# Kernel tuning notes

Measured on AMD Instinct MI355X. Metric: run time of the kernel, lower is better.

Reference implementation:

```python
import jax, jax.numpy as jnp
import numpy as np

N = 50000      # nodes
E = 1600000    # edges (avg degree 32)
F = 64         # input node features
H = 128        # GAT hidden dim (heads=1)
A = 16         # action dim
ED = 2         # edge feature dim


def setup_inputs() -> dict:
    key = jax.random.key(0)
    ks = jax.random.split(key, 20)
    def w(k, shape, fan_in):
        return jax.random.normal(k, shape, jnp.float32) * (1.0 / np.sqrt(fan_in))
    return {
        "x": jax.random.normal(ks[0], (N, F), jnp.float32),
        "edge_index": jax.random.randint(ks[1], (2, E), 0, N, dtype=jnp.int32),
        "edge_attr": jax.random.normal(ks[2], (E, ED), jnp.float32),
        # GATConv layer 1 (F -> H)
        "W1": w(ks[3], (F, H), F),
        "We1": w(ks[4], (ED, H), ED),
        "asrc1": w(ks[5], (H,), H),
        "adst1": w(ks[6], (H,), H),
        "aedge1": w(ks[7], (H,), H),
        "b1": jnp.zeros((H,), jnp.float32),
        # GATConv layer 2 (H -> H)
        "W2": w(ks[8], (H, H), H),
        "We2": w(ks[9], (ED, H), ED),
        "asrc2": w(ks[10], (H,), H),
        "adst2": w(ks[11], (H,), H),
        "aedge2": w(ks[12], (H,), H),
        "b2": jnp.zeros((H,), jnp.float32),
        # final head
        "Wfc": w(ks[13], (H, A), H),
        "bfc": jnp.zeros((A,), jnp.float32),
    }


def _gat_layer(x, src, dst, ea, W, We, a_s, a_d, a_e, b, n):
    """PyG GATConv, heads=1: gather -> attn logits -> segment softmax -> scatter-add."""
    h = x @ W                      # [n, H]
    he = ea @ We                   # [E', H]
    logits = jax.nn.leaky_relu(
        (h * a_s).sum(-1)[src] + (h * a_d).sum(-1)[dst] + (he * a_e).sum(-1),
        negative_slope=0.2,
    )                              # [E']
    m = jax.ops.segment_max(logits, dst, num_segments=n)
    p = jnp.exp(logits - m[dst])
    denom = jax.ops.segment_sum(p, dst, num_segments=n)
    alpha = p / (denom[dst] + 1e-16)
    out = jax.ops.segment_sum(h[src] * alpha[:, None], dst, num_segments=n)
    return out + b


def reference(x, edge_index, edge_attr, W1, We1, asrc1, adst1, aedge1, b1,
              W2, We2, asrc2, adst2, aedge2, b2, Wfc, bfc):
    n = x.shape[0]
    src0, dst0 = edge_index[0], edge_index[1]
    # add_self_loops=True with fill_value='mean': self-loop edge_attr is the
    # mean of incoming edge_attr per destination node (0 if no incoming edges)
    cnt = jax.ops.segment_sum(jnp.ones_like(dst0, dtype=edge_attr.dtype), dst0, num_segments=n)
    ea_mean = jax.ops.segment_sum(edge_attr, dst0, num_segments=n) / jnp.maximum(cnt, 1.0)[:, None]
    loops = jnp.arange(n, dtype=src0.dtype)
    src = jnp.concatenate([src0, loops])
    dst = jnp.concatenate([dst0, loops])
    ea = jnp.concatenate([edge_attr, ea_mean], axis=0)

    h = jax.nn.relu(_gat_layer(x, src, dst, ea, W1, We1, asrc1, adst1, aedge1, b1, n))
    h = jax.nn.relu(_gat_layer(h, src, dst, ea, W2, We2, asrc2, adst2, aedge2, b2, n))
    pooled = h.mean(axis=0)        # [H]
    return jnp.tanh(pooled @ Wfc + bfc)
```

## Files before the change

kernel.cpp:

```cpp
#include <hip/hip_runtime.h>
#include <math.h>

#define H_DIM 128
#define BWID 128
#define BMAX 512
#define CHUNK 4096

typedef int v4i __attribute__((ext_vector_type(4)));

__global__ void prep_kernel(const float* __restrict__ We1, const float* __restrict__ ae1,
                            const float* __restrict__ We2, const float* __restrict__ ae2,
                            const float* __restrict__ W1, const float* __restrict__ as1,
                            const float* __restrict__ ad1,
                            const float* __restrict__ W2, const float* __restrict__ as2,
                            const float* __restrict__ ad2,
                            float* __restrict__ c, float* __restrict__ vs1,
                            float* __restrict__ vd1, float* __restrict__ vs2,
                            float* __restrict__ vd2) {
    int t = threadIdx.x;
    if (t < 64) {
        float s = 0.f, d = 0.f;
        for (int h = 0; h < 128; ++h) {
            float w = W1[t * 128 + h];
            s += w * as1[h];
            d += w * ad1[h];
        }
        vs1[t] = s; vd1[t] = d;
    } else if (t < 192) {
        int k = t - 64;
        float s = 0.f, d = 0.f;
        for (int h = 0; h < 128; ++h) {
            float w = W2[k * 128 + h];
            s += w * as2[h];
            d += w * ad2[h];
        }
        vs2[k] = s; vd2[k] = d;
    } else {
        int l = t - 192;
        float a1x = ae1[l], a1y = ae1[l + 64];
        float a2x = ae2[l], a2y = ae2[l + 64];
        float v0 = We1[l] * a1x + We1[l + 64] * a1y;
        float v1 = We1[128 + l] * a1x + We1[192 + l] * a1y;
        float v2 = We2[l] * a2x + We2[l + 64] * a2y;
        float v3 = We2[128 + l] * a2x + We2[192 + l] * a2y;
        for (int off = 32; off; off >>= 1) {
            v0 += __shfl_xor(v0, off);
            v1 += __shfl_xor(v1, off);
            v2 += __shfl_xor(v2, off);
            v3 += __shfl_xor(v3, off);
        }
        if (l == 0) { c[0] = v0; c[1] = v1; c[2] = v2; c[3] = v3; }
    }
}

__global__ __launch_bounds__(256) void count_kernel(const int* __restrict__ ei,
                                                    int* __restrict__ gcnt, int E, int B) {
    __shared__ int hist[BMAX];
    int tid = threadIdx.x;
    for (int i = tid; i < B; i += 256) hist[i] = 0;
    __syncthreads();
    int lo = blockIdx.x * CHUNK, hi = min(lo + CHUNK, E);
    for (int e = lo + tid; e < hi; e += 256)
        atomicAdd(&hist[ei[E + e] >> 7], 1);
    __syncthreads();
    for (int i = tid; i < B; i += 256)
        if (hist[i]) atomicAdd(&gcnt[i], hist[i]);
}

__global__ void bscan_kernel(const int* __restrict__ gcnt, int* __restrict__ bstart,
                             int* __restrict__ gcur, int* __restrict__ rowptr,
                             int B, int n, int E) {
    __shared__ int s[BMAX];
    int t = threadIdx.x;
    int v0 = (t < B) ? gcnt[t] : 0;
    s[t] = v0;
    __syncthreads();
    for (int off = 1; off < BMAX; off <<= 1) {
        int v = (t >= off) ? s[t - off] : 0;
        __syncthreads();
        s[t] += v;
        __syncthreads();
    }
    if (t < B) {
        int excl = s[t] - v0;
        bstart[t] = excl;
        gcur[t] = excl;
    }
    if (t == 0) { bstart[B] = E; rowptr[n] = E; }
}

__global__ __launch_bounds__(256) void bin_kernel(const int* __restrict__ ei,
                                                  const float* __restrict__ ea,
                                                  const float* __restrict__ cvec,
                                                  int* __restrict__ gcur,
                                                  int4* __restrict__ binned, int E, int B) {
    __shared__ int cnt[BMAX];
    __shared__ int base[BMAX];
    int tid = threadIdx.x;
    for (int i = tid; i < B; i += 256) cnt[i] = 0;
    __syncthreads();
    int lo = blockIdx.x * CHUNK, hi = min(lo + CHUNK, E);
    for (int e = lo + tid; e < hi; e += 256)
        atomicAdd(&cnt[ei[E + e] >> 7], 1);
    __syncthreads();
    for (int i = tid; i < B; i += 256) {
        int c = cnt[i];
        base[i] = c ? atomicAdd(&gcur[i], c) : 0;
        cnt[i] = 0;
    }
    __syncthreads();
    float c0 = cvec[0], c1 = cvec[1], c2 = cvec[2], c3 = cvec[3];
    for (int e = lo + tid; e < hi; e += 256) {
        int s = ei[e], d = ei[E + e];
        float2 v = ((const float2*)ea)[e];
        float d1 = c0 * v.x + c1 * v.y;
        float d2 = c2 * v.x + c3 * v.y;
        int b = d >> 7;
        int loc = atomicAdd(&cnt[b], 1);
        binned[(size_t)(base[b] + loc)] = make_int4(s, d, __float_as_int(d1), __float_as_int(d2));
    }
}

__global__ __launch_bounds__(256) void build_kernel(const int* __restrict__ bstart,
                                                    const int4* __restrict__ binned,
                                                    int* __restrict__ rowptr,
                                                    int4* __restrict__ csr, int n) {
    __shared__ int cnt[BWID];
    __shared__ int sc[BWID];
    __shared__ int cur[BWID];
    int b = blockIdx.x, tid = threadIdx.x;
    int d0 = b << 7;
    int lo = bstart[b], hi = bstart[b + 1];
    if (tid < BWID) cnt[tid] = 0;
    __syncthreads();
    for (int k = lo + tid; k < hi; k += 256)
        atomicAdd(&cnt[binned[k].y & (BWID - 1)], 1);
    __syncthreads();
    if (tid < BWID) sc[tid] = cnt[tid];
    __syncthreads();
    for (int off = 1; off < BWID; off <<= 1) {
        int v = (tid < BWID && tid >= off) ? sc[tid - off] : 0;
        __syncthreads();
        if (tid < BWID) sc[tid] += v;
        __syncthreads();
    }
    if (tid < BWID) {
        int excl = sc[tid] - cnt[tid];
        cur[tid] = lo + excl;
        int d = d0 + tid;
        if (d < n) rowptr[d] = lo + excl;
    }
    __syncthreads();
    for (int k = lo + tid; k < hi; k += 256) {
        int4 e = binned[k];
        int slot = atomicAdd(&cur[e.y & (BWID - 1)], 1);
        csr[slot] = make_int4(e.x, e.z, e.w, 0);
    }
}

__global__ void hshd64_kernel(const float* __restrict__ x, const float* __restrict__ vs,
                              const float* __restrict__ vd, float* __restrict__ hs,
                              float* __restrict__ hd, int n) {
    int w = (blockIdx.x * blockDim.x + threadIdx.x) >> 6;
    int lane = threadIdx.x & 63;
    if (w >= n) return;
    float xv = x[(size_t)w * 64 + lane];
    float ss = xv * vs[lane];
    float sd = xv * vd[lane];
    for (int off = 32; off; off >>= 1) {
        ss += __shfl_xor(ss, off);
        sd += __shfl_xor(sd, off);
    }
    if (lane == 0) { hs[w] = ss; hd[w] = sd; }
}

__global__ __launch_bounds__(256) void agg64_kernel(
        const int* __restrict__ rowptr, const int4* __restrict__ csr,
        const float* __restrict__ hs, const float* __restrict__ hd,
        const float* __restrict__ feat, float* __restrict__ t_out, int n) {
    int w = (blockIdx.x * blockDim.x + threadIdx.x) >> 6;
    int lane = threadIdx.x & 63;
    if (w >= n) return;
    int beg = rowptr[w], end = rowptr[w + 1];
    int len = end - beg;
    float hdv = hd[w], hsw = hs[w];
    int g = lane >> 4;
    int c16 = lane & 15;
    float4 acc = make_float4(0.f, 0.f, 0.f, 0.f);
    float m, scale, lself;

    if (len <= 64) {
        bool valid = lane < len;
        int4 c4 = valid ? csr[beg + lane] : make_int4(0, 0, 0, 0);
        float ed = valid ? __int_as_float(c4.y) : 0.f;
        float l = hs[c4.x] + hdv + ed;
        l = (l >= 0.f) ? l : 0.2f * l;
        float mymax = valid ? l : -1e30f;
        float edsum = ed;
        for (int off = 32; off; off >>= 1) {
            mymax = fmaxf(mymax, __shfl_xor(mymax, off));
            edsum += __shfl_xor(edsum, off);
        }
        lself = hsw + hdv + edsum / fmaxf((float)len, 1.0f);
        lself = (lself >= 0.f) ? lself : 0.2f * lself;
        m = fmaxf(mymax, lself);
        float p = valid ? __expf(l - m) : 0.f;
        float psum = p;
        for (int off = 32; off; off >>= 1) psum += __shfl_xor(psum, off);
        psum += __expf(lself - m);
        scale = 1.f / (psum + 1e-16f);
        float pn = p * scale;
        int src = c4.x;
        for (int j = g; j < len; j += 4) {
            float a = __shfl(pn, j);
            int sj = __shfl(src, j);
            const float4 hv = *(const float4*)&feat[(size_t)sj * 64 + c16 * 4];
            acc.x += a * hv.x; acc.y += a * hv.y; acc.z += a * hv.z; acc.w += a * hv.w;
        }
    } else {
        float mymax = -1e30f, edsum = 0.f;
        for (int base = beg; base < end; base += 64) {
            int k = base + lane;
            if (k < end) {
                int4 c4 = csr[k];
                float ed = __int_as_float(c4.y);
                edsum += ed;
                float l = hs[c4.x] + hdv + ed;
                l = (l >= 0.f) ? l : 0.2f * l;
                mymax = fmaxf(mymax, l);
            }
        }
        for (int off = 32; off; off >>= 1) {
            mymax = fmaxf(mymax, __shfl_xor(mymax, off));
            edsum += __shfl_xor(edsum, off);
        }
        lself = hsw + hdv + edsum / fmaxf((float)len, 1.0f);
        lself = (lself >= 0.f) ? lself : 0.2f * lself;
        m = fmaxf(mymax, lself);
        float psum = 0.f;
        for (int base = beg; base < end; base += 64) {
            int k = base + lane;
            if (k < end) {
                int4 c4 = csr[k];
                float l = hs[c4.x] + hdv + __int_as_float(c4.y);
                l = (l >= 0.f) ? l : 0.2f * l;
                psum += __expf(l - m);
            }
        }
        for (int off = 32; off; off >>= 1) psum += __shfl_xor(psum, off);
        psum += __expf(lself - m);
        scale = 1.f / (psum + 1e-16f);
        for (int base = beg; base < end; base += 64) {
            int k = base + lane;
            float pn = 0.f; int src = 0;
            if (k < end) {
                int4 c4 = csr[k];
                float l = hs[c4.x] + hdv + __int_as_float(c4.y);
                l = (l >= 0.f) ? l : 0.2f * l;
                pn = __expf(l - m) * scale;
                src = c4.x;
            }
            int cl = min(end - base, 64);
            for (int j = g; j < cl; j += 4) {
                float a = __shfl(pn, j);
                int sj = __shfl(src, j);
                const float4 hv = *(const float4*)&feat[(size_t)sj * 64 + c16 * 4];
                acc.x += a * hv.x; acc.y += a * hv.y; acc.z += a * hv.z; acc.w += a * hv.w;
            }
        }
    }
    if (g == 0) {
        float a = __expf(lself - m) * scale;
        const float4 hv = *(const float4*)&feat[(size_t)w * 64 + c16 * 4];
        acc.x += a * hv.x; acc.y += a * hv.y; acc.z += a * hv.z; acc.w += a * hv.w;
    }
    float4 p1, p2, p3;
    p1.x = __shfl(acc.x, c16 + 16); p1.y = __shfl(acc.y, c16 + 16);
    p1.z = __shfl(acc.z, c16 + 16); p1.w = __shfl(acc.w, c16 + 16);
    p2.x = __shfl(acc.x, c16 + 32); p2.y = __shfl(acc.y, c16 + 32);
    p2.z = __shfl(acc.z, c16 + 32); p2.w = __shfl(acc.w, c16 + 32);
    p3.x = __shfl(acc.x, c16 + 48); p3.y = __shfl(acc.y, c16 + 48);
    p3.z = __shfl(acc.z, c16 + 48); p3.w = __shfl(acc.w, c16 + 48);
    if (lane < 16) {
        float4 o;
        o.x = acc.x + p1.x + p2.x + p3.x;
        o.y = acc.y + p1.y + p2.y + p3.y;
        o.z = acc.z + p1.z + p2.z + p3.z;
        o.w = acc.w + p1.w + p2.w + p3.w;
        *(float4*)&t_out[(size_t)w * 64 + c16 * 4] = o;
    }
}

__global__ __launch_bounds__(256) void agg128_kernel(
        const int* __restrict__ rowptr, const int4* __restrict__ csr,
        const float* __restrict__ hs, const float* __restrict__ hd,
        const float* __restrict__ feat, float* __restrict__ t_out, int n) {
    int w = (blockIdx.x * blockDim.x + threadIdx.x) >> 6;
    int lane = threadIdx.x & 63;
    if (w >= n) return;
    int beg = rowptr[w], end = rowptr[w + 1];
    int len = end - beg;
    float hdv = hd[w], hsw = hs[w];
    int half = lane >> 5;
    int col = lane & 31;
    float4 acc = make_float4(0.f, 0.f, 0.f, 0.f);
    float m, scale, lself;

    if (len <= 64) {
        bool valid = lane < len;
        int4 c4 = valid ? csr[beg + lane] : make_int4(0, 0, 0, 0);
        float ed = valid ? __int_as_float(c4.z) : 0.f;
        float l = hs[c4.x] + hdv + ed;
        l = (l >= 0.f) ? l : 0.2f * l;
        float mymax = valid ? l : -1e30f;
        float edsum = ed;
        for (int off = 32; off; off >>= 1) {
            mymax = fmaxf(mymax, __shfl_xor(mymax, off));
            edsum += __shfl_xor(edsum, off);
        }
        lself = hsw + hdv + edsum / fmaxf((float)len, 1.0f);
        lself = (lself >= 0.f) ? lself : 0.2f * lself;
        m = fmaxf(mymax, lself);
        float p = valid ? __expf(l - m) : 0.f;
        float psum = p;
        for (int off = 32; off; off >>= 1) psum += __shfl_xor(psum, off);
        psum += __expf(lself - m);
        scale = 1.f / (psum + 1e-16f);
        float pn = p * scale;
        int src = c4.x;
        for (int j = half; j < len; j += 2) {
            float a = __shfl(pn, j);
            int sj = __shfl(src, j);
            const float4 hv = *(const float4*)&feat[(size_t)sj * H_DIM + col * 4];
            acc.x += a * hv.x; acc.y += a * hv.y; acc.z += a * hv.z; acc.w += a * hv.w;
        }
    } else {
        float mymax = -1e30f, edsum = 0.f;
        for (int base = beg; base < end; base += 64) {
            int k = base + lane;
            if (k < end) {
                int4 c4 = csr[k];
                float ed = __int_as_float(c4.z);
                edsum += ed;
                float l = hs[c4.x] + hdv + ed;
                l = (l >= 0.f) ? l : 0.2f * l;
                mymax = fmaxf(mymax, l);
            }
        }
        for (int off = 32; off; off >>= 1) {
            mymax = fmaxf(mymax, __shfl_xor(mymax, off));
            edsum += __shfl_xor(edsum, off);
        }
        lself = hsw + hdv + edsum / fmaxf((float)len, 1.0f);
        lself = (lself >= 0.f) ? lself : 0.2f * lself;
        m = fmaxf(mymax, lself);
        float psum = 0.f;
        for (int base = beg; base < end; base += 64) {
            int k = base + lane;
            if (k < end) {
                int4 c4 = csr[k];
                float l = hs[c4.x] + hdv + __int_as_float(c4.z);
                l = (l >= 0.f) ? l : 0.2f * l;
                psum += __expf(l - m);
            }
        }
        for (int off = 32; off; off >>= 1) psum += __shfl_xor(psum, off);
        psum += __expf(lself - m);
        scale = 1.f / (psum + 1e-16f);
        for (int base = beg; base < end; base += 64) {
            int k = base + lane;
            float pn = 0.f; int src = 0;
            if (k < end) {
                int4 c4 = csr[k];
                float l = hs[c4.x] + hdv + __int_as_float(c4.z);
                l = (l >= 0.f) ? l : 0.2f * l;
                pn = __expf(l - m) * scale;
                src = c4.x;
            }
            int cl = min(end - base, 64);
            for (int j = half; j < cl; j += 2) {
                float a = __shfl(pn, j);
                int sj = __shfl(src, j);
                const float4 hv = *(const float4*)&feat[(size_t)sj * H_DIM + col * 4];
                acc.x += a * hv.x; acc.y += a * hv.y; acc.z += a * hv.z; acc.w += a * hv.w;
            }
        }
    }
    if (half == 0) {
        float a = __expf(lself - m) * scale;
        const float4 hv = *(const float4*)&feat[(size_t)w * H_DIM + col * 4];
        acc.x += a * hv.x; acc.y += a * hv.y; acc.z += a * hv.z; acc.w += a * hv.w;
    }
    float4 oth;
    oth.x = __shfl(acc.x, col + 32);
    oth.y = __shfl(acc.y, col + 32);
    oth.z = __shfl(acc.z, col + 32);
    oth.w = __shfl(acc.w, col + 32);
    if (half == 0) {
        float4 o;
        o.x = acc.x + oth.x; o.y = acc.y + oth.y;
        o.z = acc.z + oth.z; o.w = acc.w + oth.w;
        *(float4*)&t_out[(size_t)w * H_DIM + col * 4] = o;
    }
}

template <int FIN, bool DO_HSHD>
__global__ __launch_bounds__(256) void gemm_kernel(const float* __restrict__ X,
                                                   const float* __restrict__ W,
                                                   const float* __restrict__ bias,
                                                   const float* __restrict__ vs,
                                                   const float* __restrict__ vd,
                                                   float* __restrict__ Hout,
                                                   float* __restrict__ hs,
                                                   float* __restrict__ hd, int n) {
    __shared__ float xs[32 * FIN];
    int tid = threadIdx.x;
    int r0 = blockIdx.x * 32;
    for (int idx = tid; idx < 32 * FIN; idx += 256) {
        int r = idx / FIN, k = idx - r * FIN;
        int row = r0 + r;
        xs[idx] = (row < n) ? X[(size_t)row * FIN + k] : 0.0f;
    }
    __syncthreads();
    int tcol = tid & 31;
    int trow = tid >> 5;
    float acc[4][4] = {{0.f}};
    const float* wp = W + tcol * 4;
    const float* x0p = &xs[(trow * 4 + 0) * FIN];
    const float* x1p = &xs[(trow * 4 + 1) * FIN];
    const float* x2p = &xs[(trow * 4 + 2) * FIN];
    const float* x3p = &xs[(trow * 4 + 3) * FIN];
#pragma unroll 8
    for (int k = 0; k < FIN; ++k) {
        float4 w4 = *(const float4*)(wp + k * H_DIM);
        float x0 = x0p[k], x1 = x1p[k], x2 = x2p[k], x3 = x3p[k];
        acc[0][0] += x0 * w4.x; acc[0][1] += x0 * w4.y; acc[0][2] += x0 * w4.z; acc[0][3] += x0 * w4.w;
        acc[1][0] += x1 * w4.x; acc[1][1] += x1 * w4.y; acc[1][2] += x1 * w4.z; acc[1][3] += x1 * w4.w;
        acc[2][0] += x2 * w4.x; acc[2][1] += x2 * w4.y; acc[2][2] += x2 * w4.z; acc[2][3] += x2 * w4.w;
        acc[3][0] += x3 * w4.x; acc[3][1] += x3 * w4.y; acc[3][2] += x3 * w4.z; acc[3][3] += x3 * w4.w;
    }
    float4 b4 = *(const float4*)&bias[tcol * 4];
    float4 vs4, vd4;
    if (DO_HSHD) {
        vs4 = *(const float4*)&vs[tcol * 4];
        vd4 = *(const float4*)&vd[tcol * 4];
    }
#pragma unroll
    for (int r = 0; r < 4; ++r) {
        int row = r0 + trow * 4 + r;
        float4 o;
        o.x = fmaxf(acc[r][0] + b4.x, 0.f);
        o.y = fmaxf(acc[r][1] + b4.y, 0.f);
        o.z = fmaxf(acc[r][2] + b4.z, 0.f);
        o.w = fmaxf(acc[r][3] + b4.w, 0.f);
        if (row < n) *(float4*)&Hout[(size_t)row * H_DIM + tcol * 4] = o;
        if (DO_HSHD) {
            float ss = o.x * vs4.x + o.y * vs4.y + o.z * vs4.z + o.w * vs4.w;
            float sd = o.x * vd4.x + o.y * vd4.y + o.z * vd4.z + o.w * vd4.w;
            for (int off = 16; off; off >>= 1) {
                ss += __shfl_xor(ss, off);
                sd += __shfl_xor(sd, off);
            }
            if (tcol == 0 && row < n) { hs[row] = ss; hd[row] = sd; }
        }
    }
}

__global__ void pool_kernel(const float* __restrict__ hmat, float* __restrict__ pooled,
                            int n) {
    __shared__ float red[256];
    int col = threadIdx.x & 127;
    int half = threadIdx.x >> 7;
    int rows_per_block = (n + gridDim.x - 1) / gridDim.x;
    int r0 = blockIdx.x * rows_per_block;
    int r1 = min(r0 + rows_per_block, n);
    float s = 0.f;
    for (int r = r0 + half; r < r1; r += 2) s += hmat[(size_t)r * H_DIM + col];
    red[threadIdx.x] = s;
    __syncthreads();
    if (half == 0) atomicAdd(&pooled[col], red[threadIdx.x] + red[threadIdx.x + 128]);
}

__global__ void final_kernel(const float* __restrict__ pooled, const float* __restrict__ Wfc,
                             const float* __restrict__ bfc, float* __restrict__ out, int n) {
    int t = threadIdx.x;
    if (t >= 16) return;
    float inv_n = 1.0f / (float)n;
    float s = 0.f;
    for (int j = 0; j < 128; ++j) s += pooled[j] * inv_n * Wfc[j * 16 + t];
    out[t] = tanhf(s + bfc[t]);
}

extern "C" void kernel_launch(void* const* d_in, const int* in_sizes, int n_in,
                              void* d_out, int out_size, void* d_ws, size_t ws_size,
                              hipStream_t stream) {
    const float* x   = (const float*)d_in[0];
    const int*   ei  = (const int*)d_in[1];
    const float* ea  = (const float*)d_in[2];
    const float* W1  = (const float*)d_in[3];
    const float* We1 = (const float*)d_in[4];
    const float* as1 = (const float*)d_in[5];
    const float* ad1 = (const float*)d_in[6];
    const float* ae1 = (const float*)d_in[7];
    const float* b1  = (const float*)d_in[8];
    const float* W2  = (const float*)d_in[9];
    const float* We2 = (const float*)d_in[10];
    const float* as2 = (const float*)d_in[11];
    const float* ad2 = (const float*)d_in[12];
    const float* ae2 = (const float*)d_in[13];
    const float* b2  = (const float*)d_in[14];
    const float* Wfc = (const float*)d_in[15];
    const float* bfc = (const float*)d_in[16];
    float* out = (float*)d_out;

    const int n = in_sizes[0] / 64;
    const int E = in_sizes[1] / 2;
    const int B = (n + BWID - 1) / BWID;

    size_t o = 0;
    auto alloc = [&](size_t count) { size_t r = o; o += (count + 63) & ~(size_t)63; return r; };
    size_t o_gcnt   = alloc(BMAX);
    size_t o_bstart = alloc(BMAX + 1);
    size_t o_gcur   = alloc(BMAX);
    size_t o_rowptr = alloc(n + 1);
    size_t o_csr    = alloc(4 * (size_t)E);
    size_t o_hs     = alloc(n);
    size_t o_hd     = alloc(n);
    size_t o_bufA   = alloc((size_t)n * H_DIM);
    size_t o_bufB   = alloc((size_t)n * H_DIM);
    size_t o_c      = alloc(4);
    size_t o_vs1    = alloc(64);
    size_t o_vd1    = alloc(64);
    size_t o_vs2    = alloc(128);
    size_t o_vd2    = alloc(128);
    size_t o_pool   = alloc(128);
    (void)ws_size;
    int4* binned = (int4*)((float*)d_ws + o_bufA);

    float* wsf = (float*)d_ws;
    hipMemsetAsync(wsf + o_gcnt, 0, BMAX * sizeof(int), stream);
    hipMemsetAsync(wsf + o_pool, 0, 128 * sizeof(float), stream);

    prep_kernel<<<1, 256, 0, stream>>>(We1, ae1, We2, ae2, W1, as1, ad1, W2, as2, ad2,
        wsf + o_c, wsf + o_vs1, wsf + o_vd1, wsf + o_vs2, wsf + o_vd2);

    int ebg = (E + CHUNK - 1) / CHUNK;
    count_kernel<<<ebg, 256, 0, stream>>>(ei, (int*)(wsf + o_gcnt), E, B);
    bscan_kernel<<<1, BMAX, 0, stream>>>((int*)(wsf + o_gcnt), (int*)(wsf + o_bstart),
        (int*)(wsf + o_gcur), (int*)(wsf + o_rowptr), B, n, E);
    bin_kernel<<<ebg, 256, 0, stream>>>(ei, ea, wsf + o_c, (int*)(wsf + o_gcur),
        binned, E, B);
    build_kernel<<<B, 256, 0, stream>>>((int*)(wsf + o_bstart), binned,
        (int*)(wsf + o_rowptr), (int4*)(wsf + o_csr), n);

    int wgrid = (n + 3) / 4;

    hshd64_kernel<<<wgrid, 256, 0, stream>>>(x, wsf + o_vs1, wsf + o_vd1,
        wsf + o_hs, wsf + o_hd, n);
    agg64_kernel<<<wgrid, 256, 0, stream>>>((int*)(wsf + o_rowptr), (const int4*)(wsf + o_csr),
        wsf + o_hs, wsf + o_hd, x, wsf + o_bufB, n);
    gemm_kernel<64, true><<<(n + 31) / 32, 256, 0, stream>>>(wsf + o_bufB, W1, b1,
        wsf + o_vs2, wsf + o_vd2, wsf + o_bufA, wsf + o_hs, wsf + o_hd, n);

    agg128_kernel<<<wgrid, 256, 0, stream>>>((int*)(wsf + o_rowptr), (const int4*)(wsf + o_csr),
        wsf + o_hs, wsf + o_hd, wsf + o_bufA, wsf + o_bufB, n);
    gemm_kernel<128, false><<<(n + 31) / 32, 256, 0, stream>>>(wsf + o_bufB, W2, b2,
        nullptr, nullptr, wsf + o_bufA, nullptr, nullptr, n);

    pool_kernel<<<256, 256, 0, stream>>>(wsf + o_bufA, wsf + o_pool, n);
    final_kernel<<<1, 64, 0, stream>>>(wsf + o_pool, Wfc, bfc, out, n);
}
```

Before: 445.9 us.

## Split layer-2 aggregation into column passes with precomputed attention weights

```diff
diff --git a/kernel.cpp b/kernel.cpp
--- a/kernel.cpp
+++ b/kernel.cpp
@@ -402,6 +402,159 @@
         o.z = acc.z + oth.z; o.w = acc.w + oth.w;
         *(float4*)&t_out[(size_t)w * H_DIM + col * 4] = o;
     }
+}
+
+__global__ __launch_bounds__(256) void agg128a_kernel(
+        const int* __restrict__ rowptr, const int4* __restrict__ csr,
+        const float* __restrict__ hs, const float* __restrict__ hd,
+        const float* __restrict__ feat, float* __restrict__ t_out,
+        uint2* __restrict__ apack, float* __restrict__ aself, int n) {
+    int w = (blockIdx.x * blockDim.x + threadIdx.x) >> 6;
+    int lane = threadIdx.x & 63;
+    if (w >= n) return;
+    int beg = rowptr[w], end = rowptr[w + 1];
+    int len = end - beg;
+    float hdv = hd[w], hsw = hs[w];
+    int half = lane >> 5;
+    int c32 = lane & 31;
+    float acc = 0.f;
+    float m, scale, lself;
+
+    if (len <= 64) {
+        bool valid = lane < len;
+        int4 c4 = valid ? csr[beg + lane] : make_int4(0, 0, 0, 0);
+        float ed = valid ? __int_as_float(c4.z) : 0.f;
+        float l = hs[c4.x] + hdv + ed;
+        l = (l >= 0.f) ? l : 0.2f * l;
+        float mymax = valid ? l : -1e30f;
+        float edsum = ed;
+        for (int off = 32; off; off >>= 1) {
+            mymax = fmaxf(mymax, __shfl_xor(mymax, off));
+            edsum += __shfl_xor(edsum, off);
+        }
+        lself = hsw + hdv + edsum / fmaxf((float)len, 1.0f);
+        lself = (lself >= 0.f) ? lself : 0.2f * lself;
+        m = fmaxf(mymax, lself);
+        float p = valid ? __expf(l - m) : 0.f;
+        float psum = p;
+        for (int off = 32; off; off >>= 1) psum += __shfl_xor(psum, off);
+        psum += __expf(lself - m);
+        scale = 1.f / (psum + 1e-16f);
+        float pn = p * scale;
+        int src = c4.x;
+        if (valid) apack[beg + lane] = make_uint2((unsigned)src, (unsigned)__float_as_int(pn));
+        for (int j = half; j < len; j += 2) {
+            float a = __shfl(pn, j);
+            int sj = __shfl(src, j);
+            acc += a * feat[(size_t)sj * H_DIM + c32];
+        }
+    } else {
+        float mymax = -1e30f, edsum = 0.f;
+        for (int base = beg; base < end; base += 64) {
+            int k = base + lane;
+            if (k < end) {
+                int4 c4 = csr[k];
+                float ed = __int_as_float(c4.z);
+                edsum += ed;
+                float l = hs[c4.x] + hdv + ed;
+                l = (l >= 0.f) ? l : 0.2f * l;
+                mymax = fmaxf(mymax, l);
+            }
+        }
+        for (int off = 32; off; off >>= 1) {
+            mymax = fmaxf(mymax, __shfl_xor(mymax, off));
+            edsum += __shfl_xor(edsum, off);
+        }
+        lself = hsw + hdv + edsum / fmaxf((float)len, 1.0f);
+        lself = (lself >= 0.f) ? lself : 0.2f * lself;
+        m = fmaxf(mymax, lself);
+        float psum = 0.f;
+        for (int base = beg; base < end; base += 64) {
+            int k = base + lane;
+            if (k < end) {
+                int4 c4 = csr[k];
+                float l = hs[c4.x] + hdv + __int_as_float(c4.z);
+                l = (l >= 0.f) ? l : 0.2f * l;
+                psum += __expf(l - m);
+            }
+        }
+        for (int off = 32; off; off >>= 1) psum += __shfl_xor(psum, off);
+        psum += __expf(lself - m);
+        scale = 1.f / (psum + 1e-16f);
+        for (int base = beg; base < end; base += 64) {
+            int k = base + lane;
+            float pn = 0.f; int src = 0;
+            if (k < end) {
+                int4 c4 = csr[k];
+                float l = hs[c4.x] + hdv + __int_as_float(c4.z);
+                l = (l >= 0.f) ? l : 0.2f * l;
+                pn = __expf(l - m) * scale;
+                src = c4.x;
+                apack[k] = make_uint2((unsigned)src, (unsigned)__float_as_int(pn));
+            }
+            int cl = min(end - base, 64);
+            for (int j = half; j < cl; j += 2) {
+                float a = __shfl(pn, j);
+                int sj = __shfl(src, j);
+                acc += a * feat[(size_t)sj * H_DIM + c32];
+            }
+        }
+    }
+    float aslf = __expf(lself - m) * scale;
+    if (lane == 0) aself[w] = aslf;
+    if (half == 0)
+        acc += aslf * feat[(size_t)w * H_DIM + c32];
+    float oth = __shfl(acc, c32 + 32);
+    if (half == 0)
+        t_out[(size_t)w * H_DIM + c32] = acc + oth;
+}
+
+__global__ __launch_bounds__(256) void agg128b_kernel(
+        const int* __restrict__ rowptr, const uint2* __restrict__ apack,
+        const float* __restrict__ aself, const float* __restrict__ feat,
+        float* __restrict__ t_out, int colbase, int n) {
+    int w = (blockIdx.x * blockDim.x + threadIdx.x) >> 6;
+    int lane = threadIdx.x & 63;
+    if (w >= n) return;
+    int beg = rowptr[w], end = rowptr[w + 1];
+    int len = end - beg;
+    int half = lane >> 5;
+    int c32 = lane & 31;
+    const float* fcol = feat + colbase + c32;
+    float acc = 0.f;
+
+    if (len <= 64) {
+        bool valid = lane < len;
+        uint2 e = valid ? apack[beg + lane] : make_uint2(0u, 0u);
+        int src = (int)e.x;
+        float pn = __int_as_float((int)e.y);
+        for (int j = half; j < len; j += 2) {
+            float a = __shfl(pn, j);
+            int sj = __shfl(src, j);
+            acc += a * fcol[(size_t)sj * H_DIM];
+        }
+    } else {
+        for (int base = beg; base < end; base += 64) {
+            int k = base + lane;
+            float pn = 0.f; int src = 0;
+            if (k < end) {
+                uint2 e = apack[k];
+                src = (int)e.x;
+                pn = __int_as_float((int)e.y);
+            }
+            int cl = min(end - base, 64);
+            for (int j = half; j < cl; j += 2) {
+                float a = __shfl(pn, j);
+                int sj = __shfl(src, j);
+                acc += a * fcol[(size_t)sj * H_DIM];
+            }
+        }
+    }
+    if (half == 0)
+        acc += aself[w] * fcol[(size_t)w * H_DIM];
+    float oth = __shfl(acc, c32 + 32);
+    if (half == 0)
+        t_out[(size_t)w * H_DIM + colbase + c32] = acc + oth;
 }
 
 template <int FIN, bool DO_HSHD>
@@ -534,7 +687,9 @@
     size_t o_vs2    = alloc(128);
     size_t o_vd2    = alloc(128);
     size_t o_pool   = alloc(128);
-    (void)ws_size;
+    size_t o_apack  = alloc(2 * (size_t)E);
+    size_t o_aself  = alloc(n);
+    bool split = (o * sizeof(float) <= ws_size);
     int4* binned = (int4*)((float*)d_ws + o_bufA);
 
     float* wsf = (float*)d_ws;
@@ -562,8 +717,19 @@
     gemm_kernel<64, true><<<(n + 31) / 32, 256, 0, stream>>>(wsf + o_bufB, W1, b1,
         wsf + o_vs2, wsf + o_vd2, wsf + o_bufA, wsf + o_hs, wsf + o_hd, n);
 
-    agg128_kernel<<<wgrid, 256, 0, stream>>>((int*)(wsf + o_rowptr), (const int4*)(wsf + o_csr),
-        wsf + o_hs, wsf + o_hd, wsf + o_bufA, wsf + o_bufB, n);
+    if (split) {
+        agg128a_kernel<<<wgrid, 256, 0, stream>>>((int*)(wsf + o_rowptr),
+            (const int4*)(wsf + o_csr), wsf + o_hs, wsf + o_hd, wsf + o_bufA,
+            wsf + o_bufB, (uint2*)(wsf + o_apack), wsf + o_aself, n);
+        for (int p = 1; p < 4; ++p)
+            agg128b_kernel<<<wgrid, 256, 0, stream>>>((int*)(wsf + o_rowptr),
+                (const uint2*)(wsf + o_apack), wsf + o_aself, wsf + o_bufA,
+                wsf + o_bufB, p * 32, n);
+    } else {
+        agg128_kernel<<<wgrid, 256, 0, stream>>>((int*)(wsf + o_rowptr),
+            (const int4*)(wsf + o_csr), wsf + o_hs, wsf + o_hd, wsf + o_bufA,
+            wsf + o_bufB, n);
+    }
     gemm_kernel<128, false><<<(n + 31) / 32, 256, 0, stream>>>(wsf + o_bufB, W2, b2,
         nullptr, nullptr, wsf + o_bufA, nullptr, nullptr, n);
 
```

New measurement: 545.4 us. +22.3%, slower.
